# Kernel tuning notes

Hardware: AMD Instinct MI355X
Metric: run time of the kernel (lower is better)

The kernel has to match this reference:

```python
import jax, jax.numpy as jnp
import numpy as np

B, S, D, H = 2, 1024, 768, 12
HD = D // H          # head_dim = 64
DFF = 4 * D          # 3072
EPS = 1e-5


def _ln(x, g, b):
    m = x.mean(-1, keepdims=True)
    v = ((x - m) ** 2).mean(-1, keepdims=True)
    return (x - m) * jax.lax.rsqrt(v + EPS) * g + b


def setup_inputs() -> dict:
    key = jax.random.key(0)
    ks = jax.random.split(key, 8)
    w = lambda k, shape: jax.random.normal(k, shape, jnp.float32) * 0.02
    return {
        "inp": jax.random.normal(ks[0], (B, S, D), jnp.float32),
        "attention_mask": jnp.zeros((B, S), bool),  # True = masked out (filled with -inf)
        "rel_matrix": jax.random.randint(ks[1], (B, S, S), -1, 2, jnp.int32),  # values in {-1,0,1}
        "qkv_w": w(ks[2], (3 * D, D)),
        "rel_A": w(ks[3], (3, HD)),        # relative_position_emb_A.weight
        "o_w": w(ks[4], (D, D)),
        "w1": w(ks[5], (DFF, D)), "b1": jnp.zeros((DFF,), jnp.float32),
        "w2": w(ks[6], (D, DFF)), "b2": jnp.zeros((D,), jnp.float32),
        "ln1_g": jnp.ones((D,), jnp.float32), "ln1_b": jnp.zeros((D,), jnp.float32),
        "ln2_g": jnp.ones((D,), jnp.float32), "ln2_b": jnp.zeros((D,), jnp.float32),
    }


def reference(inp, attention_mask, rel_matrix, qkv_w, rel_A, o_w,
              w1, b1, w2, b2, ln1_g, ln1_b, ln2_g, ln2_b):
    x = _ln(inp, ln1_g, ln1_b)
    qkv = x @ qkv_w.T                                  # (B,S,3D)
    q, k, v = jnp.split(qkv, 3, axis=-1)
    heads = lambda t: t.reshape(B, S, H, HD).transpose(0, 2, 1, 3)  # (B,H,S,HD)
    q, k, v = heads(q), heads(k), heads(v)

    # q @ (k + rel_emb)^T without materializing k_aug:
    # q.k^T term plus per-(q,key) relative term gathered from q @ A^T.
    logits = jnp.einsum("bhqd,bhkd->bhqk", q, k)       # (B,H,S,S)
    r = jnp.einsum("bhqd,cd->bhqc", q, rel_A)          # (B,H,S,3)
    idx = (rel_matrix + 1).astype(jnp.int32)           # (B,S,S) in {0,1,2}
    rel = jnp.take_along_axis(r, jnp.broadcast_to(idx[:, None], (B, H, S, S)), axis=-1)
    logits = (logits + rel) / np.sqrt(HD).astype(np.float32)
    # masked_fill: -inf where mask is True
    logits = jnp.where(attention_mask[:, None, None, :], -jnp.inf, logits)

    attn = jax.nn.softmax(logits, axis=-1)
    out = jnp.einsum("bhqk,bhkd->bhqd", attn, v)
    out = out.transpose(0, 2, 1, 3).reshape(B, S, D)
    inp = inp + out @ o_w.T                            # residual (dropout=0)

    h = _ln(inp, ln2_g, ln2_b)
    mlp = jax.nn.relu(h @ w1.T + b1) @ w2.T + b2
    return inp + mlp
```

## Files before the change

kernel.cpp:

```cpp
#include <hip/hip_runtime.h>
#include <hip/hip_bf16.h>

#define BB 2
#define SS 1024
#define DD 768
#define HH 12
#define HD 64
#define DFF 3072
#define EPS 1e-5f
#define BS2 (BB * SS)
#define BSD ((size_t)BS2 * DD)

typedef unsigned short ushort_t;
typedef unsigned char uchar_t;
using short8 = __attribute__((ext_vector_type(8))) short;
using f32x4  = __attribute__((ext_vector_type(4))) float;

#define WAITCNT_LGKM0 0xC07F

__device__ __forceinline__ ushort_t f2bf_rne(float f) {
    union { float f; unsigned u; } x; x.f = f;
    unsigned r = x.u + 0x7fff + ((x.u >> 16) & 1);
    return (ushort_t)(r >> 16);
}
__device__ __forceinline__ float bf2f(short u) {
    union { unsigned i; float f; } x;
    x.i = ((unsigned)(ushort_t)u) << 16;
    return x.f;
}

#define CVT_N1 (3 * DD * DD / 4)
#define CVT_N2 (CVT_N1 + DD * DD / 4)
#define CVT_N3 (CVT_N2 + DFF * DD / 4)
#define CVT_NT (CVT_N3 + DD * DFF / 4)
#define PREP_CVT   (CVT_NT / 256)
#define PREP_CODES (BB * SS)
#define PREP_LN    BS2

__global__ __launch_bounds__(256) void prep_kernel(
    const float* __restrict__ qkv_w, const float* __restrict__ o_w,
    const float* __restrict__ w1, const float* __restrict__ w2,
    ushort_t* __restrict__ wdst,
    const int* __restrict__ rel, const uchar_t* __restrict__ mask,
    unsigned* __restrict__ codes,
    const float* __restrict__ x, const float* __restrict__ g,
    const float* __restrict__ b, ushort_t* __restrict__ y)
{
    const int bx = blockIdx.x;
    const int t  = threadIdx.x;
    if (bx < PREP_CVT) {
        int i = bx * 256 + t;
        const float* src; int off;
        if (i < CVT_N1)      { src = qkv_w; off = i; }
        else if (i < CVT_N2) { src = o_w;   off = i - CVT_N1; }
        else if (i < CVT_N3) { src = w1;    off = i - CVT_N2; }
        else                 { src = w2;    off = i - CVT_N3; }
        float4 v = ((const float4*)src)[off];
        ushort4 o;
        o.x = f2bf_rne(v.x); o.y = f2bf_rne(v.y);
        o.z = f2bf_rne(v.z); o.w = f2bf_rne(v.w);
        ((ushort4*)wdst)[i] = o;
        return;
    }
    if (bx < PREP_CVT + PREP_CODES) {
        int tid = (bx - PREP_CVT) * 256 + t;
        int l15 = tid & 15;
        int kt  = (tid >> 4) & 15;
        int q   = (tid >> 8) & (SS - 1);
        int bb  = tid >> 18;
        const int* rrow = rel + ((size_t)(bb * SS + q)) * SS + kt * 64 + l15;
        const uchar_t* mrow = mask + (size_t)bb * SS + kt * 64 + l15;
        unsigned o = 0;
#pragma unroll
        for (int nt = 0; nt < 4; ++nt) {
            unsigned c = mrow[nt * 16] ? 3u : (unsigned)(rrow[nt * 16] + 1);
            o |= c << (8 * nt);
        }
        codes[((size_t)(bb * SS + q) * 16 + kt) * 16 + l15] = o;
        return;
    }
    const int row = bx - PREP_CVT - PREP_CODES;
    const float* xr = x + (size_t)row * DD;
    float s = 0.f, ss = 0.f;
    for (int i = t; i < DD; i += 256) {
        float v = xr[i];
        s += v; ss += v * v;
    }
    for (int off = 32; off; off >>= 1) {
        s  += __shfl_down(s,  off);
        ss += __shfl_down(ss, off);
    }
    __shared__ float reds[4], redss[4], bc[2];
    if ((t & 63) == 0) { reds[t >> 6] = s; redss[t >> 6] = ss; }
    __syncthreads();
    if (t == 0) {
        float S1 = reds[0] + reds[1] + reds[2] + reds[3];
        float S2 = redss[0] + redss[1] + redss[2] + redss[3];
        float mean = S1 / DD;
        float var = S2 / DD - mean * mean;
        bc[0] = mean;
        bc[1] = rsqrtf(var + EPS);
    }
    __syncthreads();
    float mean = bc[0], inv = bc[1];
    ushort_t* yr = y + (size_t)row * DD;
    for (int i = t; i < DD; i += 256) {
        yr[i] = f2bf_rne((xr[i] - mean) * inv * g[i] + b[i]);
    }
}

__global__ __launch_bounds__(256) void merge2_ln_kernel(
    const ushort_t* __restrict__ part, const float* __restrict__ inp,
    const float* __restrict__ g, const float* __restrict__ b,
    float* __restrict__ resid, ushort_t* __restrict__ h_bf)
{
    const int row = blockIdx.x;
    const int t = threadIdx.x;
    float4 v = make_float4(0.f, 0.f, 0.f, 0.f);
    const size_t idx = (size_t)row * (DD / 4) + t;
    if (t < DD / 4) {
        v = ((const float4*)inp)[idx];
        ushort4 p0 = ((const ushort4*)part)[idx];
        ushort4 p1 = ((const ushort4*)(part + BSD))[idx];
        v.x += bf2f(p0.x) + bf2f(p1.x);
        v.y += bf2f(p0.y) + bf2f(p1.y);
        v.z += bf2f(p0.z) + bf2f(p1.z);
        v.w += bf2f(p0.w) + bf2f(p1.w);
        ((float4*)resid)[idx] = v;
    }
    float s  = v.x + v.y + v.z + v.w;
    float ss = v.x * v.x + v.y * v.y + v.z * v.z + v.w * v.w;
    for (int off = 32; off; off >>= 1) {
        s  += __shfl_down(s,  off);
        ss += __shfl_down(ss, off);
    }
    __shared__ float reds[4], redss[4], bc[2];
    if ((t & 63) == 0) { reds[t >> 6] = s; redss[t >> 6] = ss; }
    __syncthreads();
    if (t == 0) {
        float S1 = reds[0] + reds[1] + reds[2] + reds[3];
        float S2 = redss[0] + redss[1] + redss[2] + redss[3];
        float mean = S1 / DD;
        float var = S2 / DD - mean * mean;
        bc[0] = mean;
        bc[1] = rsqrtf(var + EPS);
    }
    __syncthreads();
    if (t < DD / 4) {
        const float mean = bc[0], inv = bc[1];
        float4 gv = ((const float4*)g)[t];
        float4 bv = ((const float4*)b)[t];
        ushort4 o;
        o.x = f2bf_rne((v.x - mean) * inv * gv.x + bv.x);
        o.y = f2bf_rne((v.y - mean) * inv * gv.y + bv.y);
        o.z = f2bf_rne((v.z - mean) * inv * gv.z + bv.z);
        o.w = f2bf_rne((v.w - mean) * inv * gv.w + bv.w);
        ((ushort4*)h_bf)[idx] = o;
    }
}

__global__ __launch_bounds__(256) void merge4_kernel(
    const ushort_t* __restrict__ part, const float* __restrict__ resid,
    const float* __restrict__ b2, float* __restrict__ outp, int n4)
{
    int i = blockIdx.x * 256 + threadIdx.x;
    if (i >= n4) return;
    float4 v = ((const float4*)resid)[i];
    int col4 = (i * 4) % DD;
    float4 bv = *(const float4*)(b2 + col4);
    v.x += bv.x; v.y += bv.y; v.z += bv.z; v.w += bv.w;
#pragma unroll
    for (int z = 0; z < 4; ++z) {
        ushort4 pz = ((const ushort4*)(part + (size_t)z * BSD))[i];
        v.x += bf2f(pz.x); v.y += bf2f(pz.y);
        v.z += bf2f(pz.z); v.w += bf2f(pz.w);
    }
    ((float4*)outp)[i] = v;
}

template <bool RELU, bool OUT_BF16, bool HAS_BIAS, bool PARTIAL>
__global__ __launch_bounds__(256) void gemm_tile(
    const ushort_t* __restrict__ A, const ushort_t* __restrict__ W,
    const float* __restrict__ bias, void* __restrict__ Cout,
    int M, int N, int K, int Ksplit, int nx)
{
    __shared__ __align__(16) ushort_t As[512 * 8];
    __shared__ __align__(16) ushort_t Bs[1024 * 8];

    const int nwg = gridDim.x;
    const int swz = (blockIdx.x & 7) * (nwg >> 3) + (blockIdx.x >> 3);
    const int by  = swz & 31;
    const int t2  = swz >> 5;
    const int bxx = t2 % nx;
    const int bz  = t2 / nx;

    const int t  = threadIdx.x;
    const int n0 = bxx * 128;
    const int m0 = by * 64;
    const int kb = bz * Ksplit;
    const int w  = t >> 6;
    const int l  = t & 63;
    const int wm = (w & 1) * 32;
    const int wn = (w >> 1) * 64;
    const int l15  = l & 15;
    const int quad = l >> 4;

    const ushort_t* gA = A + (size_t)(m0 + (t & 63)) * K + kb + (t >> 6) * 8;
    const ushort_t* gB = W + (size_t)(n0 + (t & 127)) * K + kb + (t >> 7) * 8;

    short8 pa0 = *(const short8*)(gA);
    short8 pa1 = *(const short8*)(gA + 32);
    short8 pb0 = *(const short8*)(gB);
    short8 pb1 = *(const short8*)(gB + 16);
    short8 pb2 = *(const short8*)(gB + 32);
    short8 pb3 = *(const short8*)(gB + 48);

    f32x4 acc[2][4] = {};
    const int nIter = Ksplit >> 6;

    for (int it = 0; it < nIter; ++it) {
        __builtin_amdgcn_s_barrier();
        *(short8*)&As[(size_t)t * 8]           = pa0;
        *(short8*)&As[(size_t)(t + 256) * 8]   = pa1;
        *(short8*)&Bs[(size_t)t * 8]           = pb0;
        *(short8*)&Bs[(size_t)(t + 256) * 8]   = pb1;
        *(short8*)&Bs[(size_t)(t + 512) * 8]   = pb2;
        *(short8*)&Bs[(size_t)(t + 768) * 8]   = pb3;
        if (it + 1 < nIter) {
            const int k0 = (it + 1) << 6;
            pa0 = *(const short8*)(gA + k0);
            pa1 = *(const short8*)(gA + k0 + 32);
            pb0 = *(const short8*)(gB + k0);
            pb1 = *(const short8*)(gB + k0 + 16);
            pb2 = *(const short8*)(gB + k0 + 32);
            pb3 = *(const short8*)(gB + k0 + 48);
        }
        __builtin_amdgcn_s_waitcnt(WAITCNT_LGKM0);
        __builtin_amdgcn_s_barrier();

#pragma unroll
        for (int ks = 0; ks < 2; ++ks) {
            const ushort_t* aptr = &As[(size_t)((ks * 4 + quad) * 64 + wm + l15) * 8];
            const ushort_t* bptr = &Bs[(size_t)((ks * 4 + quad) * 128 + wn + l15) * 8];
            short8 af[2], bf[4];
#pragma unroll
            for (int i = 0; i < 2; ++i)
                af[i] = *(const short8*)(aptr + (size_t)i * 16 * 8);
#pragma unroll
            for (int j = 0; j < 4; ++j)
                bf[j] = *(const short8*)(bptr + (size_t)j * 16 * 8);
#pragma unroll
            for (int i = 0; i < 2; ++i)
#pragma unroll
                for (int j = 0; j < 4; ++j)
                    acc[i][j] = __builtin_amdgcn_mfma_f32_16x16x32_bf16(
                        af[i], bf[j], acc[i][j], 0, 0, 0);
        }
    }

    if (PARTIAL) {
        ushort_t* Cp = (ushort_t*)Cout + (size_t)bz * ((size_t)M * N);
#pragma unroll
        for (int i = 0; i < 2; ++i) {
            const int row = m0 + wm + i * 16 + quad * 4;
#pragma unroll
            for (int j = 0; j < 4; ++j) {
                const int col = n0 + wn + j * 16 + l15;
#pragma unroll
                for (int r = 0; r < 4; ++r)
                    Cp[(size_t)(row + r) * N + col] = f2bf_rne(acc[i][j][r]);
            }
        }
    } else {
#pragma unroll
        for (int i = 0; i < 2; ++i) {
            const int row = m0 + wm + i * 16 + quad * 4;
#pragma unroll
            for (int j = 0; j < 4; ++j) {
                const int col = n0 + wn + j * 16 + l15;
                const float bv = HAS_BIAS ? bias[col] : 0.f;
#pragma unroll
                for (int r = 0; r < 4; ++r) {
                    float v = acc[i][j][r] + bv;
                    if (RELU) v = fmaxf(v, 0.f);
                    if (OUT_BF16)
                        ((ushort_t*)Cout)[(size_t)(row + r) * N + col] = f2bf_rne(v);
                    else
                        ((float*)Cout)[(size_t)(row + r) * N + col] = v;
                }
            }
        }
    }
}

__global__ __launch_bounds__(256) void attn_mfma_kernel(
    const ushort_t* __restrict__ qkv,
    const unsigned* __restrict__ codes,
    const float* __restrict__ rel_A,
    ushort_t* __restrict__ Opart,
    float* __restrict__ lpart)
{
    __shared__ __align__(16) ushort_t Ks[2][64 * 64];
    __shared__ __align__(16) unsigned Vt2[2][64 * 36];
    __shared__ __align__(16) ushort_t Ps[64 * 72];
    __shared__ __align__(16) float r3s[64][4];

    const int bx = blockIdx.x;
    const int ks = bx & 1;
    const int qt = (bx >> 1) & 15;
    const int h  = (bx >> 5) % HH;
    const int b  = bx / (32 * HH);
    const int q0 = qt * 64;
    const int t  = threadIdx.x;
    const int w  = t >> 6;
    const int l  = t & 63;
    const int l15  = l & 15;
    const int quad = l >> 4;

    const int sr  = t >> 3;
    const int scp = t & 7;
    const int vkp = t >> 3;
    const int vdg = t & 7;
    const int vkps = vkp ^ (vdg * 4);

    const size_t qrow = (size_t)(b * SS + q0 + w * 16 + l15) * (3 * DD) + h * HD;
    const short8 qf0 = *(const short8*)(qkv + qrow + quad * 8);
    const short8 qf1 = *(const short8*)(qkv + qrow + 32 + quad * 8);

    {
        float rv[3];
#pragma unroll
        for (int c = 0; c < 3; ++c) {
            const float* a = rel_A + c * HD + quad * 8;
            float acc = 0.f;
#pragma unroll
            for (int j = 0; j < 8; ++j) acc += bf2f(qf0[j]) * a[j];
#pragma unroll
            for (int j = 0; j < 8; ++j) acc += bf2f(qf1[j]) * a[32 + j];
            acc += __shfl_xor(acc, 16);
            acc += __shfl_xor(acc, 32);
            rv[c] = acc;
        }
        if (quad == 0) {
            float4 f4 = make_float4(rv[0], rv[1], rv[2], -2.4e31f);
            *(float4*)&r3s[w * 16 + l15][0] = f4;
        }
    }

    float l_run[4] = {0.f, 0.f, 0.f, 0.f};
    f32x4 oacc[4] = {};

    const int kt0 = ks * 8;
    short8 va, vb;
    {
        const int k0 = kt0 * 64;
        const int cl  = scp ^ (sr & 7);
        const ushort_t* g = qkv + (size_t)(b * SS + k0 + sr) * (3 * DD) + DD + h * HD + cl * 8;
        __builtin_amdgcn_global_load_lds(
            (const __attribute__((address_space(1))) unsigned*)g,
            (__attribute__((address_space(3))) unsigned*)(&Ks[0][0] + (size_t)t * 8), 16, 0, 0);
        const int r2  = sr + 32;
        const int cl2 = scp ^ (r2 & 7);
        const ushort_t* g2 = qkv + (size_t)(b * SS + k0 + r2) * (3 * DD) + DD + h * HD + cl2 * 8;
        __builtin_amdgcn_global_load_lds(
            (const __attribute__((address_space(1))) unsigned*)g2,
            (__attribute__((address_space(3))) unsigned*)(&Ks[0][0] + (size_t)(t + 256) * 8), 16, 0, 0);
        const ushort_t* gv = qkv + (size_t)(b * SS + k0 + 2 * vkp) * (3 * DD) + 2 * DD + h * HD + vdg * 8;
        va = *(const short8*)gv;
        vb = *(const short8*)(gv + 3 * DD);
#pragma unroll
        for (int i = 0; i < 8; ++i)
            Vt2[0][(size_t)(vdg * 8 + i) * 36 + vkps] =
                (unsigned)(ushort_t)va[i] | ((unsigned)(ushort_t)vb[i] << 16);
    }
    __syncthreads();
    float4 r3v[4];
#pragma unroll
    for (int reg = 0; reg < 4; ++reg)
        r3v[reg] = *(const float4*)&r3s[w * 16 + quad * 4 + reg][0];

    for (int i8 = 0; i8 < 8; ++i8) {
        const int kt  = kt0 + i8;
        const int cur = i8 & 1;
        const bool more = (i8 + 1 < 8);
        if (more) {
            const int k0 = (kt + 1) * 64;
            const int nb = cur ^ 1;
            const int cl  = scp ^ (sr & 7);
            const ushort_t* g = qkv + (size_t)(b * SS + k0 + sr) * (3 * DD) + DD + h * HD + cl * 8;
            __builtin_amdgcn_global_load_lds(
                (const __attribute__((address_space(1))) unsigned*)g,
                (__attribute__((address_space(3))) unsigned*)(&Ks[nb][0] + (size_t)t * 8), 16, 0, 0);
            const int r2  = sr + 32;
            const int cl2 = scp ^ (r2 & 7);
            const ushort_t* g2 = qkv + (size_t)(b * SS + k0 + r2) * (3 * DD) + DD + h * HD + cl2 * 8;
            __builtin_amdgcn_global_load_lds(
                (const __attribute__((address_space(1))) unsigned*)g2,
                (__attribute__((address_space(3))) unsigned*)(&Ks[nb][0] + (size_t)(t + 256) * 8), 16, 0, 0);
            const ushort_t* gv = qkv + (size_t)(b * SS + k0 + 2 * vkp) * (3 * DD) + 2 * DD + h * HD + vdg * 8;
            va = *(const short8*)gv;
            vb = *(const short8*)(gv + 3 * DD);
        }

        f32x4 sacc[4] = {};
#pragma unroll
        for (int kc = 0; kc < 2; ++kc) {
            const short8 qv = kc ? qf1 : qf0;
#pragma unroll
            for (int nt = 0; nt < 4; ++nt) {
                const int row = nt * 16 + l15;
                const int cp  = (kc * 4 + quad) ^ (row & 7);
                const short8 kf = *(const short8*)(&Ks[cur][0] + (size_t)row * 64 + cp * 8);
                sacc[nt] = __builtin_amdgcn_mfma_f32_16x16x32_bf16(qv, kf, sacc[nt], 0, 0, 0);
            }
        }

#pragma unroll
        for (int reg = 0; reg < 4; ++reg) {
            const int qloc = w * 16 + quad * 4 + reg;
            const unsigned cds = codes[((size_t)(b * SS + q0 + qloc) * 16 + kt) * 16 + l15];
            const float4 r4 = r3v[reg];
#pragma unroll
            for (int nt = 0; nt < 4; ++nt) {
                const unsigned c = (cds >> (8 * nt)) & 0xff;
                float rvv = (c == 0) ? r4.x : (c == 1) ? r4.y : (c == 2) ? r4.z : r4.w;
                const float p = __expf((sacc[nt][reg] + rvv) * 0.125f);
                l_run[reg] += p;
                Ps[(size_t)qloc * 72 + nt * 16 + l15] = f2bf_rne(p);
            }
        }

#pragma unroll
        for (int kc = 0; kc < 2; ++kc) {
            const short8 pf = *(const short8*)(Ps + (size_t)(w * 16 + l15) * 72 + kc * 32 + quad * 8);
#pragma unroll
            for (int dt = 0; dt < 4; ++dt) {
                const int d  = dt * 16 + l15;
                const int dg = d >> 3;
                const int kps0 = (kc * 16 + quad * 4) ^ ((dg & 7) * 4);
                const short8 vf = *(const short8*)((const ushort_t*)&Vt2[cur][(size_t)d * 36 + kps0]);
                oacc[dt] = __builtin_amdgcn_mfma_f32_16x16x32_bf16(pf, vf, oacc[dt], 0, 0, 0);
            }
        }

        if (more) {
            const int nb = cur ^ 1;
#pragma unroll
            for (int i = 0; i < 8; ++i)
                Vt2[nb][(size_t)(vdg * 8 + i) * 36 + vkps] =
                    (unsigned)(ushort_t)va[i] | ((unsigned)(ushort_t)vb[i] << 16);
            __syncthreads();
        }
    }

    ushort_t* Op = Opart + (size_t)ks * BSD;
    float* lp = lpart + (size_t)ks * BS2 * HH;
#pragma unroll
    for (int reg = 0; reg < 4; ++reg) {
        float ls = l_run[reg];
        ls += __shfl_xor(ls, 1);
        ls += __shfl_xor(ls, 2);
        ls += __shfl_xor(ls, 4);
        ls += __shfl_xor(ls, 8);
        const int orow = b * SS + q0 + w * 16 + quad * 4 + reg;
#pragma unroll
        for (int dt = 0; dt < 4; ++dt)
            Op[(size_t)orow * DD + h * HD + dt * 16 + l15] = f2bf_rne(oacc[dt][reg]);
        if (l15 == 0) lp[(size_t)orow * HH + h] = ls;
    }
}

__global__ __launch_bounds__(256) void attn_merge(
    const ushort_t* __restrict__ Opart, const float* __restrict__ lpart,
    ushort_t* __restrict__ att_bf)
{
    int i = blockIdx.x * 256 + threadIdx.x;
    int row = (i * 4) / DD;
    int h   = ((i * 4) % DD) >> 6;
    float l0 = lpart[(size_t)row * HH + h];
    float l1 = lpart[(size_t)BS2 * HH + (size_t)row * HH + h];
    float inv = 1.0f / (l0 + l1);
    ushort4 a = ((const ushort4*)Opart)[i];
    ushort4 b = ((const ushort4*)(Opart + BSD))[i];
    ushort4 o;
    o.x = f2bf_rne((bf2f(a.x) + bf2f(b.x)) * inv);
    o.y = f2bf_rne((bf2f(a.y) + bf2f(b.y)) * inv);
    o.z = f2bf_rne((bf2f(a.z) + bf2f(b.z)) * inv);
    o.w = f2bf_rne((bf2f(a.w) + bf2f(b.w)) * inv);
    ((ushort4*)att_bf)[i] = o;
}

extern "C" void kernel_launch(void* const* d_in, const int* in_sizes, int n_in,
                              void* d_out, int out_size, void* d_ws, size_t ws_size,
                              hipStream_t stream) {
    const float* inp   = (const float*)d_in[0];
    const uchar_t* amask = (const uchar_t*)d_in[1];
    const int*   relm  = (const int*)d_in[2];
    const float* qkv_w = (const float*)d_in[3];
    const float* rel_A = (const float*)d_in[4];
    const float* o_w   = (const float*)d_in[5];
    const float* w1    = (const float*)d_in[6];
    const float* b1    = (const float*)d_in[7];
    const float* w2    = (const float*)d_in[8];
    const float* b2    = (const float*)d_in[9];
    const float* ln1_g = (const float*)d_in[10];
    const float* ln1_b = (const float*)d_in[11];
    const float* ln2_g = (const float*)d_in[12];
    const float* ln2_b = (const float*)d_in[13];
    float* out = (float*)d_out;

    char* p = (char*)d_ws;
    ushort_t* x_bf   = (ushort_t*)p; p += BSD * 2;
    ushort_t* att_bf = (ushort_t*)p; p += BSD * 2;
    ushort_t* h_bf   = (ushort_t*)p; p += BSD * 2;
    ushort_t* ff_bf  = (ushort_t*)p; p += (size_t)BS2 * DFF * 2;
    ushort_t* qkvw_bf= (ushort_t*)p; p += (size_t)3 * DD * DD * 2;
    ushort_t* ow_bf  = (ushort_t*)p; p += (size_t)DD * DD * 2;
    ushort_t* w1_bf  = (ushort_t*)p; p += (size_t)DFF * DD * 2;
    ushort_t* w2_bf  = (ushort_t*)p; p += (size_t)DD * DFF * 2;
    ushort_t* qkv_bf = (ushort_t*)p; p += (size_t)BS2 * 3 * DD * 2;
    float*    resid  = (float*)p;    p += BSD * 4;
    ushort_t* pool   = (ushort_t*)p; p += 4 * BSD * 2;
    ushort_t* Opart  = (ushort_t*)p; p += 2 * BSD * 2;
    float*    lpart  = (float*)p;    p += (size_t)2 * BS2 * HH * 4;
    unsigned* codes  = (unsigned*)p; p += (size_t)BB * SS * SS;

    prep_kernel<<<PREP_CVT + PREP_CODES + PREP_LN, 256, 0, stream>>>(
        qkv_w, o_w, w1, w2, qkvw_bf, relm, amask, codes,
        inp, ln1_g, ln1_b, x_bf);

    gemm_tile<false, true, false, false>
        <<<3 * DD / 128 * 32, 256, 0, stream>>>(
        x_bf, qkvw_bf, nullptr, qkv_bf, BS2, 3 * DD, DD, DD, 3 * DD / 128);

    attn_mfma_kernel<<<BB * HH * 16 * 2, 256, 0, stream>>>(
        qkv_bf, codes, rel_A, Opart, lpart);
    attn_merge<<<(int)(BSD / 4 / 256), 256, 0, stream>>>(Opart, lpart, att_bf);

    gemm_tile<false, false, false, true>
        <<<DD / 128 * 32 * 2, 256, 0, stream>>>(
        att_bf, ow_bf, nullptr, pool, BS2, DD, DD, DD / 2, DD / 128);

    merge2_ln_kernel<<<BS2, 256, 0, stream>>>(
        pool, inp, ln2_g, ln2_b, resid, h_bf);

    gemm_tile<true, true, true, false>
        <<<DFF / 128 * 32, 256, 0, stream>>>(
        h_bf, w1_bf, b1, ff_bf, BS2, DFF, DD, DD, DFF / 128);

    gemm_tile<false, false, false, true>
        <<<DD / 128 * 32 * 4, 256, 0, stream>>>(
        ff_bf, w2_bf, nullptr, pool, BS2, DD, DFF, DFF / 4, DD / 128);

    merge4_kernel<<<(int)(BSD / 4 / 256), 256, 0, stream>>>(
        pool, resid, b2, out, (int)(BSD / 4));
}
```

Before: 253.2 us.

## Fuse attention merge into O-proj GEMM load and atomically accumulate FFN2 output

The attention partial-output merge (sum of two bf16 partials times 1/(l0+l1)) moves into the A-operand load path of the output-projection GEMM, so the separate attn_merge kernel and the att_bf buffer go away. The residual-plus-b2 base is now written straight into the output by the LN2 kernel, and the split-K FFN2 GEMM atomically adds fp32 partials into it, which removes the merge4 kernel and its bf16 partial round trip. This saves two launches and several full-tensor passes over memory. In exchange the O-proj GEMM loads twice the A data plus per-head normalizers, and FFN2 does many fp32 atomics with a non-deterministic summation order.

```diff
diff --git a/kernel.cpp b/kernel.cpp
--- a/kernel.cpp
+++ b/kernel.cpp
@@ -27,6 +27,13 @@
     union { unsigned i; float f; } x;
     x.i = ((unsigned)(ushort_t)u) << 16;
     return x.f;
+}
+__device__ __forceinline__ short8 mergeo(short8 a, short8 b, float inv) {
+    short8 o;
+#pragma unroll
+    for (int i = 0; i < 8; ++i)
+        o[i] = (short)f2bf_rne((bf2f(a[i]) + bf2f(b[i])) * inv);
+    return o;
 }
 
 #define CVT_N1 (3 * DD * DD / 4)
@@ -112,7 +119,8 @@
 __global__ __launch_bounds__(256) void merge2_ln_kernel(
     const ushort_t* __restrict__ part, const float* __restrict__ inp,
     const float* __restrict__ g, const float* __restrict__ b,
-    float* __restrict__ resid, ushort_t* __restrict__ h_bf)
+    const float* __restrict__ b2,
+    float* __restrict__ outp, ushort_t* __restrict__ h_bf)
 {
     const int row = blockIdx.x;
     const int t = threadIdx.x;
@@ -126,7 +134,11 @@
         v.y += bf2f(p0.y) + bf2f(p1.y);
         v.z += bf2f(p0.z) + bf2f(p1.z);
         v.w += bf2f(p0.w) + bf2f(p1.w);
-        ((float4*)resid)[idx] = v;
+        float4 b2v = ((const float4*)b2)[t];
+        float4 o;
+        o.x = v.x + b2v.x; o.y = v.y + b2v.y;
+        o.z = v.z + b2v.z; o.w = v.w + b2v.w;
+        ((float4*)outp)[idx] = o;
     }
     float s  = v.x + v.y + v.z + v.w;
     float ss = v.x * v.x + v.y * v.y + v.z * v.z + v.w * v.w;
@@ -159,29 +171,11 @@
     }
 }
 
-__global__ __launch_bounds__(256) void merge4_kernel(
-    const ushort_t* __restrict__ part, const float* __restrict__ resid,
-    const float* __restrict__ b2, float* __restrict__ outp, int n4)
-{
-    int i = blockIdx.x * 256 + threadIdx.x;
-    if (i >= n4) return;
-    float4 v = ((const float4*)resid)[i];
-    int col4 = (i * 4) % DD;
-    float4 bv = *(const float4*)(b2 + col4);
-    v.x += bv.x; v.y += bv.y; v.z += bv.z; v.w += bv.w;
-#pragma unroll
-    for (int z = 0; z < 4; ++z) {
-        ushort4 pz = ((const ushort4*)(part + (size_t)z * BSD))[i];
-        v.x += bf2f(pz.x); v.y += bf2f(pz.y);
-        v.z += bf2f(pz.z); v.w += bf2f(pz.w);
-    }
-    ((float4*)outp)[i] = v;
-}
-
-template <bool RELU, bool OUT_BF16, bool HAS_BIAS, bool PARTIAL>
+template <bool RELU, bool OUT_BF16, bool HAS_BIAS, bool PARTIAL, bool ATOMIC, bool FUSE_ATT>
 __global__ __launch_bounds__(256) void gemm_tile(
     const ushort_t* __restrict__ A, const ushort_t* __restrict__ W,
     const float* __restrict__ bias, void* __restrict__ Cout,
+    const float* __restrict__ lpart,
     int M, int N, int K, int Ksplit, int nx)
 {
     __shared__ __align__(16) ushort_t As[512 * 8];
@@ -208,8 +202,26 @@
     const ushort_t* gA = A + (size_t)(m0 + (t & 63)) * K + kb + (t >> 6) * 8;
     const ushort_t* gB = W + (size_t)(n0 + (t & 127)) * K + kb + (t >> 7) * 8;
 
-    short8 pa0 = *(const short8*)(gA);
-    short8 pa1 = *(const short8*)(gA + 32);
+    const float* lp0 = nullptr; const float* lp1 = nullptr;
+    const int hbase = kb >> 6;
+    if (FUSE_ATT) {
+        lp0 = lpart + (size_t)(m0 + (t & 63)) * HH;
+        lp1 = lp0 + (size_t)BS2 * HH;
+    }
+
+    short8 pa0, pa1, ra0, ra1, sa0, sa1;
+    float li0 = 0.f, li1 = 0.f;
+    if (FUSE_ATT) {
+        ra0 = *(const short8*)(gA);
+        ra1 = *(const short8*)(gA + 32);
+        sa0 = *(const short8*)(gA + BSD);
+        sa1 = *(const short8*)(gA + BSD + 32);
+        li0 = lp0[hbase];
+        li1 = lp1[hbase];
+    } else {
+        pa0 = *(const short8*)(gA);
+        pa1 = *(const short8*)(gA + 32);
+    }
     short8 pb0 = *(const short8*)(gB);
     short8 pb1 = *(const short8*)(gB + 16);
     short8 pb2 = *(const short8*)(gB + 32);
@@ -220,6 +232,11 @@
 
     for (int it = 0; it < nIter; ++it) {
         __builtin_amdgcn_s_barrier();
+        if (FUSE_ATT) {
+            const float inv = 1.0f / (li0 + li1);
+            pa0 = mergeo(ra0, sa0, inv);
+            pa1 = mergeo(ra1, sa1, inv);
+        }
         *(short8*)&As[(size_t)t * 8]           = pa0;
         *(short8*)&As[(size_t)(t + 256) * 8]   = pa1;
         *(short8*)&Bs[(size_t)t * 8]           = pb0;
@@ -228,8 +245,17 @@
         *(short8*)&Bs[(size_t)(t + 768) * 8]   = pb3;
         if (it + 1 < nIter) {
             const int k0 = (it + 1) << 6;
-            pa0 = *(const short8*)(gA + k0);
-            pa1 = *(const short8*)(gA + k0 + 32);
+            if (FUSE_ATT) {
+                ra0 = *(const short8*)(gA + k0);
+                ra1 = *(const short8*)(gA + k0 + 32);
+                sa0 = *(const short8*)(gA + k0 + BSD);
+                sa1 = *(const short8*)(gA + k0 + BSD + 32);
+                li0 = lp0[hbase + it + 1];
+                li1 = lp1[hbase + it + 1];
+            } else {
+                pa0 = *(const short8*)(gA + k0);
+                pa1 = *(const short8*)(gA + k0 + 32);
+            }
             pb0 = *(const short8*)(gB + k0);
             pb1 = *(const short8*)(gB + k0 + 16);
             pb2 = *(const short8*)(gB + k0 + 32);
@@ -269,6 +295,19 @@
 #pragma unroll
                 for (int r = 0; r < 4; ++r)
                     Cp[(size_t)(row + r) * N + col] = f2bf_rne(acc[i][j][r]);
+            }
+        }
+    } else if (ATOMIC) {
+        float* Cp = (float*)Cout;
+#pragma unroll
+        for (int i = 0; i < 2; ++i) {
+            const int row = m0 + wm + i * 16 + quad * 4;
+#pragma unroll
+            for (int j = 0; j < 4; ++j) {
+                const int col = n0 + wn + j * 16 + l15;
+#pragma unroll
+                for (int r = 0; r < 4; ++r)
+                    atomicAdd(&Cp[(size_t)(row + r) * N + col], acc[i][j][r]);
             }
         }
     } else {
@@ -470,26 +509,6 @@
     }
 }
 
-__global__ __launch_bounds__(256) void attn_merge(
-    const ushort_t* __restrict__ Opart, const float* __restrict__ lpart,
-    ushort_t* __restrict__ att_bf)
-{
-    int i = blockIdx.x * 256 + threadIdx.x;
-    int row = (i * 4) / DD;
-    int h   = ((i * 4) % DD) >> 6;
-    float l0 = lpart[(size_t)row * HH + h];
-    float l1 = lpart[(size_t)BS2 * HH + (size_t)row * HH + h];
-    float inv = 1.0f / (l0 + l1);
-    ushort4 a = ((const ushort4*)Opart)[i];
-    ushort4 b = ((const ushort4*)(Opart + BSD))[i];
-    ushort4 o;
-    o.x = f2bf_rne((bf2f(a.x) + bf2f(b.x)) * inv);
-    o.y = f2bf_rne((bf2f(a.y) + bf2f(b.y)) * inv);
-    o.z = f2bf_rne((bf2f(a.z) + bf2f(b.z)) * inv);
-    o.w = f2bf_rne((bf2f(a.w) + bf2f(b.w)) * inv);
-    ((ushort4*)att_bf)[i] = o;
-}
-
 extern "C" void kernel_launch(void* const* d_in, const int* in_sizes, int n_in,
                               void* d_out, int out_size, void* d_ws, size_t ws_size,
                               hipStream_t stream) {
@@ -511,7 +530,6 @@
 
     char* p = (char*)d_ws;
     ushort_t* x_bf   = (ushort_t*)p; p += BSD * 2;
-    ushort_t* att_bf = (ushort_t*)p; p += BSD * 2;
     ushort_t* h_bf   = (ushort_t*)p; p += BSD * 2;
     ushort_t* ff_bf  = (ushort_t*)p; p += (size_t)BS2 * DFF * 2;
     ushort_t* qkvw_bf= (ushort_t*)p; p += (size_t)3 * DD * DD * 2;
@@ -519,7 +537,6 @@
     ushort_t* w1_bf  = (ushort_t*)p; p += (size_t)DFF * DD * 2;
     ushort_t* w2_bf  = (ushort_t*)p; p += (size_t)DD * DFF * 2;
     ushort_t* qkv_bf = (ushort_t*)p; p += (size_t)BS2 * 3 * DD * 2;
-    float*    resid  = (float*)p;    p += BSD * 4;
     ushort_t* pool   = (ushort_t*)p; p += 4 * BSD * 2;
     ushort_t* Opart  = (ushort_t*)p; p += 2 * BSD * 2;
     float*    lpart  = (float*)p;    p += (size_t)2 * BS2 * HH * 4;
@@ -529,29 +546,25 @@
         qkv_w, o_w, w1, w2, qkvw_bf, relm, amask, codes,
         inp, ln1_g, ln1_b, x_bf);
 
-    gemm_tile<false, true, false, false>
+    gemm_tile<false, true, false, false, false, false>
         <<<3 * DD / 128 * 32, 256, 0, stream>>>(
-        x_bf, qkvw_bf, nullptr, qkv_bf, BS2, 3 * DD, DD, DD, 3 * DD / 128);
+        x_bf, qkvw_bf, nullptr, qkv_bf, nullptr, BS2, 3 * DD, DD, DD, 3 * DD / 128);
 
     attn_mfma_kernel<<<BB * HH * 16 * 2, 256, 0, stream>>>(
         qkv_bf, codes, rel_A, Opart, lpart);
-    attn_merge<<<(int)(BSD / 4 / 256), 256, 0, stream>>>(Opart, lpart, att_bf);
-
-    gemm_tile<false, false, false, true>
+
+    gemm_tile<false, false, false, true, false, true>
         <<<DD / 128 * 32 * 2, 256, 0, stream>>>(
-        att_bf, ow_bf, nullptr, pool, BS2, DD, DD, DD / 2, DD / 128);
+        Opart, ow_bf, nullptr, pool, lpart, BS2, DD, DD, DD / 2, DD / 128);
 
     merge2_ln_kernel<<<BS2, 256, 0, stream>>>(
-        pool, inp, ln2_g, ln2_b, resid, h_bf);
-
-    gemm_tile<true, true, true, false>
+        pool, inp, ln2_g, ln2_b, b2, out, h_bf);
+
+    gemm_tile<true, true, true, false, false, false>
         <<<DFF / 128 * 32, 256, 0, stream>>>(
-        h_bf, w1_bf, b1, ff_bf, BS2, DFF, DD, DD, DFF / 128);
-
-    gemm_tile<false, false, false, true>
+        h_bf, w1_bf, b1, ff_bf, nullptr, BS2, DFF, DD, DD, DFF / 128);
+
+    gemm_tile<false, false, false, false, true, false>
         <<<DD / 128 * 32 * 4, 256, 0, stream>>>(
-        ff_bf, w2_bf, nullptr, pool, BS2, DD, DFF, DFF / 4, DD / 128);
-
-    merge4_kernel<<<(int)(BSD / 4 / 256), 256, 0, stream>>>(
-        pool, resid, b2, out, (int)(BSD / 4));
-}
+        ff_bf, w2_bf, nullptr, out, nullptr, BS2, DD, DFF, DFF / 4, DD / 128);
+}
```

After: 263.5 us. +4.0%, slower.

## Double-buffer GEMM LDS tiles with direct global-to-LDS async loads

Applied to the files above, without the earlier changes.

Replaces the register-staged prefetch in the GEMM tile kernel with global_load_lds copies straight into LDS and a two-stage LDS double buffer. Loads for tile it+2 are issued after computing tile it, and vmcnt waits gate consumption. The aim is to drop the VGPR staging and the ds_write traffic and to overlap memory latency with MFMA work. It doubles LDS use per block, which may lower occupancy. It also depends on the 16-byte direct-to-LDS layout matching the old per-thread layout, and on the wait counts being correct.

```diff
diff --git a/kernel.cpp b/kernel.cpp
--- a/kernel.cpp
+++ b/kernel.cpp
@@ -15,8 +15,6 @@
 typedef unsigned char uchar_t;
 using short8 = __attribute__((ext_vector_type(8))) short;
 using f32x4  = __attribute__((ext_vector_type(4))) float;
-
-#define WAITCNT_LGKM0 0xC07F
 
 __device__ __forceinline__ ushort_t f2bf_rne(float f) {
     union { float f; unsigned u; } x; x.f = f;
@@ -184,8 +182,8 @@
     const float* __restrict__ bias, void* __restrict__ Cout,
     int M, int N, int K, int Ksplit, int nx)
 {
-    __shared__ __align__(16) ushort_t As[512 * 8];
-    __shared__ __align__(16) ushort_t Bs[1024 * 8];
+    __shared__ __align__(16) ushort_t As[2][512 * 8];
+    __shared__ __align__(16) ushort_t Bs[2][1024 * 8];
 
     const int nwg = gridDim.x;
     const int swz = (blockIdx.x & 7) * (nwg >> 3) + (blockIdx.x >> 3);
@@ -208,40 +206,49 @@
     const ushort_t* gA = A + (size_t)(m0 + (t & 63)) * K + kb + (t >> 6) * 8;
     const ushort_t* gB = W + (size_t)(n0 + (t & 127)) * K + kb + (t >> 7) * 8;
 
-    short8 pa0 = *(const short8*)(gA);
-    short8 pa1 = *(const short8*)(gA + 32);
-    short8 pb0 = *(const short8*)(gB);
-    short8 pb1 = *(const short8*)(gB + 16);
-    short8 pb2 = *(const short8*)(gB + 32);
-    short8 pb3 = *(const short8*)(gB + 48);
+    auto stage = [&](int buf, int k0) {
+        const ushort_t* a = gA + k0;
+        const ushort_t* b = gB + k0;
+        __builtin_amdgcn_global_load_lds(
+            (const __attribute__((address_space(1))) unsigned*)(a),
+            (__attribute__((address_space(3))) unsigned*)(&As[buf][(size_t)t * 8]), 16, 0, 0);
+        __builtin_amdgcn_global_load_lds(
+            (const __attribute__((address_space(1))) unsigned*)(a + 32),
+            (__attribute__((address_space(3))) unsigned*)(&As[buf][(size_t)(t + 256) * 8]), 16, 0, 0);
+        __builtin_amdgcn_global_load_lds(
+            (const __attribute__((address_space(1))) unsigned*)(b),
+            (__attribute__((address_space(3))) unsigned*)(&Bs[buf][(size_t)t * 8]), 16, 0, 0);
+        __builtin_amdgcn_global_load_lds(
+            (const __attribute__((address_space(1))) unsigned*)(b + 16),
+            (__attribute__((address_space(3))) unsigned*)(&Bs[buf][(size_t)(t + 256) * 8]), 16, 0, 0);
+        __builtin_amdgcn_global_load_lds(
+            (const __attribute__((address_space(1))) unsigned*)(b + 32),
+            (__attribute__((address_space(3))) unsigned*)(&Bs[buf][(size_t)(t + 512) * 8]), 16, 0, 0);
+        __builtin_amdgcn_global_load_lds(
+            (const __attribute__((address_space(1))) unsigned*)(b + 48),
+            (__attribute__((address_space(3))) unsigned*)(&Bs[buf][(size_t)(t + 768) * 8]), 16, 0, 0);
+    };
 
     f32x4 acc[2][4] = {};
     const int nIter = Ksplit >> 6;
 
+    stage(0, 0);
+    stage(1, 64);
+
     for (int it = 0; it < nIter; ++it) {
+        const int cur = it & 1;
+        if (it + 1 < nIter) {
+            asm volatile("s_waitcnt vmcnt(6)" ::: "memory");
+        } else {
+            asm volatile("s_waitcnt vmcnt(0)" ::: "memory");
+        }
+        __builtin_amdgcn_sched_barrier(0);
         __builtin_amdgcn_s_barrier();
-        *(short8*)&As[(size_t)t * 8]           = pa0;
-        *(short8*)&As[(size_t)(t + 256) * 8]   = pa1;
-        *(short8*)&Bs[(size_t)t * 8]           = pb0;
-        *(short8*)&Bs[(size_t)(t + 256) * 8]   = pb1;
-        *(short8*)&Bs[(size_t)(t + 512) * 8]   = pb2;
-        *(short8*)&Bs[(size_t)(t + 768) * 8]   = pb3;
-        if (it + 1 < nIter) {
-            const int k0 = (it + 1) << 6;
-            pa0 = *(const short8*)(gA + k0);
-            pa1 = *(const short8*)(gA + k0 + 32);
-            pb0 = *(const short8*)(gB + k0);
-            pb1 = *(const short8*)(gB + k0 + 16);
-            pb2 = *(const short8*)(gB + k0 + 32);
-            pb3 = *(const short8*)(gB + k0 + 48);
-        }
-        __builtin_amdgcn_s_waitcnt(WAITCNT_LGKM0);
-        __builtin_amdgcn_s_barrier();
 
 #pragma unroll
         for (int ks = 0; ks < 2; ++ks) {
-            const ushort_t* aptr = &As[(size_t)((ks * 4 + quad) * 64 + wm + l15) * 8];
-            const ushort_t* bptr = &Bs[(size_t)((ks * 4 + quad) * 128 + wn + l15) * 8];
+            const ushort_t* aptr = &As[cur][(size_t)((ks * 4 + quad) * 64 + wm + l15) * 8];
+            const ushort_t* bptr = &Bs[cur][(size_t)((ks * 4 + quad) * 128 + wn + l15) * 8];
             short8 af[2], bf[4];
 #pragma unroll
             for (int i = 0; i < 2; ++i)
@@ -256,6 +263,8 @@
                     acc[i][j] = __builtin_amdgcn_mfma_f32_16x16x32_bf16(
                         af[i], bf[j], acc[i][j], 0, 0, 0);
         }
+        __builtin_amdgcn_s_barrier();
+        if (it + 2 < nIter) stage(cur, (it + 2) << 6);
     }
 
     if (PARTIAL) {
```

Measured after the change: 264.8 us. +4.6%, slower.
